# Optimization experiments

Hardware: AMD Instinct MI355X
Metric: run time of the kernel (lower is better)

Reference implementation:

```python
import jax, jax.numpy as jnp
import numpy as np

B, T, D = 2, 2048, 2048
N, KH, H = 16, 8, 128  # query heads, kv heads, head_dim
S = 2048               # cache size
EPS = 1e-6
ROPE_THETA = 1000000.0
K_MASK = -0.7 * float(np.finfo(np.float32).max)  # jax _get_large_negative(float32)


def _rms_norm(x, w):
    rms = jnp.sqrt(jnp.mean(x.astype(jnp.float32) ** 2, axis=-1, keepdims=True) + EPS)
    return (w * x / rms).astype(x.dtype)


def _rope_embeddings(positions, head_dim):
    fraction = jnp.arange(0, head_dim, 2, dtype=jnp.float32) / head_dim
    inv_freq = 1.0 / (ROPE_THETA ** fraction)
    sinusoid = jnp.einsum('BT,k->BTk', positions.astype(jnp.float32), inv_freq,
                          precision=jax.lax.Precision.HIGHEST)
    return jnp.sin(sinusoid), jnp.cos(sinusoid)


def _apply_rope(x, sin, cos):
    h = x.shape[-1] // 2
    x1, x2 = x[..., :h], x[..., h:]
    s, c = sin[:, :, None, :], cos[:, :, None, :]
    return jnp.concatenate([x1 * c - x2 * s, x2 * c + x1 * s], axis=-1).astype(x.dtype)


def _positions_from_segment_ids(seg):
    t = seg.shape[1]
    pos = jnp.arange(t, dtype=jnp.int32)[None, :] - jnp.argmax(seg, axis=1)[:, None]
    return jnp.where(seg != 0, pos, 2 ** 30)


def _num_left_pad(seg):
    return jnp.sum(jnp.cumsum(seg != 0, axis=-1) == 0, axis=-1).astype(jnp.int32)


def _attention(x, q_w, k_w, v_w, o_w, q_norm_w, k_norm_w, k_cache, v_cache,
               segment_ids, start_ind, cur_ind):
    b, t, _ = x.shape
    s = k_cache.shape[1]
    n, kh, h = q_w.shape[1], k_w.shape[1], q_w.shape[2]

    q = _rms_norm(jnp.einsum('BTD,DNH->BTNH', x, q_w), q_norm_w)  # [B,T,N,H]
    k = _rms_norm(jnp.einsum('BSD,DKH->BSKH', x, k_w), k_norm_w)  # [B,T,K,H]
    v = jnp.einsum('BSD,DKH->BSKH', x, v_w)                       # [B,T,K,H]

    start = jnp.where(start_ind < 0, _num_left_pad(segment_ids), start_ind)
    pos = _positions_from_segment_ids(segment_ids) + cur_ind
    sin, cos = _rope_embeddings(pos, h)
    q = _apply_rope(q, sin, cos)
    k = _apply_rope(k, sin, cos)

    # KV-cache update at cur_ind
    k_cache = jax.lax.dynamic_update_slice(k_cache, k, (0, cur_ind, 0, 0))
    v_cache = jax.lax.dynamic_update_slice(v_cache, v, (0, cur_ind, 0, 0))

    # GQA: group query heads per kv head
    qg = q.reshape(b, t, kh, n // kh, h)
    logits = jnp.einsum('BTHGD,BSHD->BHGTS', qg, k_cache) * (h ** -0.5)

    q_pos = cur_ind + jnp.arange(t, dtype=jnp.int32)[None, :] - start[:, None]  # [B,T]
    ts = jnp.arange(s, dtype=jnp.int32)
    kv_seg = (ts[None, :] >= start[:, None]) & (ts[None, :] < cur_ind + t)      # [B,S] bool
    k_pos = ts[None, :] - start[:, None]                                        # [B,S]
    causal = k_pos[:, None, :] <= q_pos[:, :, None]                             # [B,T,S]
    # faithful to original: bool kv segment ids compared against int segment_ids
    seg_mask = kv_seg[:, None, :].astype(segment_ids.dtype) == segment_ids[:, :, None]
    final_mask = (causal & seg_mask)[:, None, None, :, :]                       # [B,1,1,T,S]

    logits = jnp.where(final_mask, logits, K_MASK)
    attn = jax.nn.softmax(logits.astype(jnp.float32), axis=-1).astype(logits.dtype)
    o = jnp.einsum('BHGTS,BSHD->BTHGD', attn, v_cache).reshape(b, t, n, h)
    return jnp.einsum('BTNH,NHD->BTD', o, o_w)


def setup_inputs() -> dict:
    key = jax.random.key(0)
    ks = jax.random.split(key, 5)
    scale = 0.02
    return {
        'x': jax.random.normal(ks[0], (B, T, D), jnp.float32),
        'q_w': jax.random.normal(ks[1], (D, N, H), jnp.float32) * scale,
        'k_w': jax.random.normal(ks[2], (D, KH, H), jnp.float32) * scale,
        'v_w': jax.random.normal(ks[3], (D, KH, H), jnp.float32) * scale,
        'o_w': jax.random.normal(ks[4], (N, H, D), jnp.float32) * scale,
        'q_norm_w': jnp.ones((H,), jnp.float32),
        'k_norm_w': jnp.ones((H,), jnp.float32),
        'k_cache': jnp.zeros((B, S, KH, H), jnp.float32),
        'v_cache': jnp.zeros((B, S, KH, H), jnp.float32),
        'segment_ids': jnp.ones((B, T), jnp.int32),
        'start_ind': jnp.zeros((B,), jnp.int32),
        'cur_ind': 0,
        'right_pads': 0,
    }


def reference(x, q_w, k_w, v_w, o_w, q_norm_w, k_norm_w, k_cache, v_cache,
              segment_ids, start_ind, cur_ind, right_pads):
    # right_pads only advances the cache write pointer (stateful side effect); it
    # does not affect the attention output.
    return _attention(x, q_w, k_w, v_w, o_w, q_norm_w, k_norm_w,
                      k_cache, v_cache, segment_ids, start_ind, cur_ind)
```

## Files before the change

### kernel.cpp

```cpp
#include <hip/hip_runtime.h>
#include <hip/hip_fp16.h>
#include <climits>
#include <math.h>

#define Bc   2
#define Tc   2048
#define Dc   2048
#define Nc   16
#define KHc  8
#define Hc   128
#define Sc   2048

constexpr float EPSc   = 1e-6f;
constexpr float SCALE2 = 0.1275174477984469f;

typedef short short8 __attribute__((ext_vector_type(8)));
typedef _Float16 half8 __attribute__((ext_vector_type(8)));
typedef __fp16 fp16x2 __attribute__((ext_vector_type(2)));
typedef float float4v __attribute__((ext_vector_type(4)));

union U16x8 { uint4 u; short8 s8; half8 h8; unsigned short us[8]; };
union H2U  { fp16x2 h; unsigned u; };
union S8H8 { short8 s; half8 h; };

__device__ __forceinline__ unsigned short f2bf(float f) {
    union { float f; unsigned u; } v; v.f = f;
    unsigned r = v.u + 0x7FFFu + ((v.u >> 16) & 1u);
    return (unsigned short)(r >> 16);
}
__device__ __forceinline__ float bf2f(unsigned short u) {
    union { unsigned u; float f; } v; v.u = ((unsigned)u) << 16;
    return v.f;
}

__device__ __forceinline__ void tc_body(const float* __restrict__ in,
                                        unsigned short* __restrict__ out,
                                        int R, int C, int bx, int by, int tid,
                                        float tile[32][33])
{
    int c0 = bx * 32, r0 = by * 32;
#pragma unroll
    for (int i = 0; i < 4; ++i) {
        int row = (tid >> 5) + i * 8, col = tid & 31;
        tile[row][col] = in[(size_t)(r0 + row) * C + c0 + col];
    }
    __syncthreads();
#pragma unroll
    for (int i = 0; i < 4; ++i) {
        int rowo = (tid >> 5) + i * 8, colo = tid & 31;
        out[(size_t)(c0 + rowo) * R + r0 + colo] = f2bf(tile[colo][rowo]);
    }
}

__global__ __launch_bounds__(256) void prep(const float* __restrict__ x,
                                            const float* __restrict__ qw,
                                            const float* __restrict__ kw,
                                            const float* __restrict__ vw,
                                            const float* __restrict__ ow,
                                            const int* __restrict__ seg,
                                            const int* __restrict__ start_ind,
                                            int* __restrict__ meta,
                                            unsigned short* __restrict__ xb,
                                            unsigned short* __restrict__ qkvwT,
                                            unsigned short* __restrict__ owT)
{
    __shared__ float tile[32][33];
    __shared__ int s_max, s_amax, s_nz;
    int id = blockIdx.x;
    int tid = threadIdx.x;

    if (id < Bc) {
        int b = id;
        if (tid == 0) { s_max = INT_MIN; s_amax = Tc; s_nz = Tc; }
        __syncthreads();
        int lmax = INT_MIN;
        for (int t = tid; t < Tc; t += 256) lmax = max(lmax, seg[b * Tc + t]);
        atomicMax(&s_max, lmax);
        __syncthreads();
        int mv = s_max;
        int lamax = Tc, lnz = Tc;
        for (int t = tid; t < Tc; t += 256) {
            int v = seg[b * Tc + t];
            if (v == mv) lamax = min(lamax, t);
            if (v != 0)  lnz   = min(lnz, t);
        }
        atomicMin(&s_amax, lamax);
        atomicMin(&s_nz, lnz);
        __syncthreads();
        if (tid == 0) {
            meta[b] = s_amax;
            int st = start_ind[b];
            meta[Bc + b] = (st < 0) ? s_nz : st;
        }
        return;
    }
    id -= Bc;
    if (id < 4096) {
        size_t base = ((size_t)id * 256 + tid) * 8;
        float4 a = *(const float4*)&x[base];
        float4 b = *(const float4*)&x[base + 4];
        U16x8 o;
        o.us[0] = f2bf(a.x); o.us[1] = f2bf(a.y); o.us[2] = f2bf(a.z); o.us[3] = f2bf(a.w);
        o.us[4] = f2bf(b.x); o.us[5] = f2bf(b.y); o.us[6] = f2bf(b.z); o.us[7] = f2bf(b.w);
        *(uint4*)&xb[base] = o.u;
        return;
    }
    id -= 4096;
    if (id < 4096) { tc_body(qw, qkvwT, 2048, 2048, id & 63, id >> 6, tid, tile); return; }
    id -= 4096;
    if (id < 2048) { tc_body(kw, qkvwT + (size_t)2048 * 2048, 2048, 1024, id & 31, id >> 5, tid, tile); return; }
    id -= 2048;
    if (id < 2048) { tc_body(vw, qkvwT + (size_t)3072 * 2048, 2048, 1024, id & 31, id >> 5, tid, tile); return; }
    id -= 2048;
    tc_body(ow, owT, 2048, 2048, id & 63, id >> 6, tid, tile);
}

__global__ __launch_bounds__(512, 2) void gemm256(const unsigned short* __restrict__ A,
                                                  const unsigned short* __restrict__ BT,
                                                  void* __restrict__ Cout,
                                                  int M, int N, int K, int out_fp32)
{
    __shared__ __align__(16) unsigned short As[2 * 16384];
    __shared__ __align__(16) unsigned short Bs[2 * 16384];

    int tid = threadIdx.x;
    int lane = tid & 63, w = tid >> 6;
    int quad = lane >> 4, l15 = lane & 15;

    int gx = gridDim.x;
    int nwg = gx * gridDim.y;
    int lin = blockIdx.y * gx + blockIdx.x;
    int swz = (lin & 7) * (nwg >> 3) + (lin >> 3);
    int bm = (swz / gx) * 256, bn = (swz % gx) * 256;

    int KT = K >> 6;

    int colswz = (((lane & 7) ^ ((lane >> 3) & 7)) << 3);
    int r0 = (w * 2) * 8 + (lane >> 3);
    const unsigned short* Ab0 = A + (size_t)(bm + r0) * K + colswz;
    const unsigned short* Bb0 = BT + (size_t)(bn + r0) * K + colswz;
    size_t rowK8 = (size_t)8 * K;
    size_t hK = (size_t)128 * K;

    unsigned short* dA0 = As + (w * 2) * 512;
    unsigned short* dB0 = Bs + (w * 2) * 512;

    auto stA = [&](int kt, int bufp) __attribute__((always_inline)) {
#pragma unroll
        for (int h = 0; h < 2; ++h) {
            __builtin_amdgcn_global_load_lds(
                (__attribute__((address_space(1))) void*)(Ab0 + h * hK + (size_t)kt * 64),
                (__attribute__((address_space(3))) void*)(dA0 + bufp * 16384 + h * 8192), 16, 0, 0);
            __builtin_amdgcn_global_load_lds(
                (__attribute__((address_space(1))) void*)(Ab0 + h * hK + rowK8 + (size_t)kt * 64),
                (__attribute__((address_space(3))) void*)(dA0 + bufp * 16384 + h * 8192 + 512), 16, 0, 0);
        }
    };
    auto stB = [&](int kt, int bufp) __attribute__((always_inline)) {
#pragma unroll
        for (int h = 0; h < 2; ++h) {
            __builtin_amdgcn_global_load_lds(
                (__attribute__((address_space(1))) void*)(Bb0 + h * hK + (size_t)kt * 64),
                (__attribute__((address_space(3))) void*)(dB0 + bufp * 16384 + h * 8192), 16, 0, 0);
            __builtin_amdgcn_global_load_lds(
                (__attribute__((address_space(1))) void*)(Bb0 + h * hK + rowK8 + (size_t)kt * 64),
                (__attribute__((address_space(3))) void*)(dB0 + bufp * 16384 + h * 8192 + 512), 16, 0, 0);
        }
    };

    int ards = (w >> 2) * 8192;
    int brds = (w & 3) * 4096;
    int rowb = l15 * 64;
    int swA = l15 & 7;
    int cof0 = ((quad) ^ swA) << 3;
    int cof1 = ((4 + quad) ^ swA) << 3;

    float4v acc[8][4];
#pragma unroll
    for (int i = 0; i < 8; ++i)
#pragma unroll
        for (int j = 0; j < 4; ++j) acc[i][j] = (float4v)0.f;

    stA(0, 0); stB(0, 0);
    stA(1, 1);
    asm volatile("s_waitcnt vmcnt(4)" ::: "memory");
    __builtin_amdgcn_s_barrier();
    asm volatile("" ::: "memory");

    auto ktile = [&](int kt, int bufp) __attribute__((always_inline)) {
        const unsigned short* ab = As + bufp * 16384 + ards + rowb;
        const unsigned short* bb = Bs + bufp * 16384 + brds + rowb;
        short8 afl[2][4], afh[2][4], bfa[2][2], bfb[2][2];

        if (kt + 1 < KT) stB(kt + 1, bufp ^ 1);
#pragma unroll
        for (int mi = 0; mi < 4; ++mi) {
            afl[0][mi] = *(const short8*)&ab[mi * 1024 + cof0];
            afl[1][mi] = *(const short8*)&ab[mi * 1024 + cof1];
        }
#pragma unroll
        for (int ni = 0; ni < 2; ++ni) {
            bfa[0][ni] = *(const short8*)&bb[ni * 1024 + cof0];
            bfa[1][ni] = *(const short8*)&bb[ni * 1024 + cof1];
        }
        __builtin_amdgcn_s_setprio(1);
#pragma unroll
        for (int kk = 0; kk < 2; ++kk)
#pragma unroll
            for (int mi = 0; mi < 4; ++mi)
#pragma unroll
                for (int ni = 0; ni < 2; ++ni)
                    acc[mi][ni] = __builtin_amdgcn_mfma_f32_16x16x32_bf16(afl[kk][mi], bfa[kk][ni], acc[mi][ni], 0, 0, 0);
        __builtin_amdgcn_s_setprio(0);
#pragma unroll
        for (int ni = 0; ni < 2; ++ni) {
            bfb[0][ni] = *(const short8*)&bb[(2 + ni) * 1024 + cof0];
            bfb[1][ni] = *(const short8*)&bb[(2 + ni) * 1024 + cof1];
        }
        __builtin_amdgcn_s_setprio(1);
#pragma unroll
        for (int kk = 0; kk < 2; ++kk)
#pragma unroll
            for (int mi = 0; mi < 4; ++mi)
#pragma unroll
                for (int ni = 0; ni < 2; ++ni)
                    acc[mi][2 + ni] = __builtin_amdgcn_mfma_f32_16x16x32_bf16(afl[kk][mi], bfb[kk][ni], acc[mi][2 + ni], 0, 0, 0);
        __builtin_amdgcn_s_setprio(0);
#pragma unroll
        for (int mi = 0; mi < 4; ++mi) {
            afh[0][mi] = *(const short8*)&ab[(4 + mi) * 1024 + cof0];
            afh[1][mi] = *(const short8*)&ab[(4 + mi) * 1024 + cof1];
        }
        asm volatile("s_waitcnt lgkmcnt(0)" ::: "memory");
        __builtin_amdgcn_sched_barrier(0);
        __builtin_amdgcn_s_barrier();
        asm volatile("" ::: "memory");

        bool sA = (kt + 2) < KT;
        if (sA) stA(kt + 2, bufp);
        __builtin_amdgcn_s_setprio(1);
#pragma unroll
        for (int kk = 0; kk < 2; ++kk)
#pragma unroll
            for (int mi = 0; mi < 4; ++mi)
#pragma unroll
                for (int ni = 0; ni < 2; ++ni)
                    acc[4 + mi][ni] = __builtin_amdgcn_mfma_f32_16x16x32_bf16(afh[kk][mi], bfa[kk][ni], acc[4 + mi][ni], 0, 0, 0);
#pragma unroll
        for (int kk = 0; kk < 2; ++kk)
#pragma unroll
            for (int mi = 0; mi < 4; ++mi)
#pragma unroll
                for (int ni = 0; ni < 2; ++ni)
                    acc[4 + mi][2 + ni] = __builtin_amdgcn_mfma_f32_16x16x32_bf16(afh[kk][mi], bfb[kk][ni], acc[4 + mi][2 + ni], 0, 0, 0);
        __builtin_amdgcn_s_setprio(0);
        if (sA) asm volatile("s_waitcnt vmcnt(4)" ::: "memory");
        else    asm volatile("s_waitcnt vmcnt(0)" ::: "memory");
        __builtin_amdgcn_sched_barrier(0);
        __builtin_amdgcn_s_barrier();
        asm volatile("" ::: "memory");
    };

    for (int kt = 0; kt < KT; kt += 2) {
        ktile(kt, 0);
        ktile(kt + 1, 1);
    }

    int wm = (w >> 2) * 128, wn = (w & 3) * 64;
#pragma unroll
    for (int mi = 0; mi < 8; ++mi)
#pragma unroll
        for (int ni = 0; ni < 4; ++ni)
#pragma unroll
            for (int reg = 0; reg < 4; ++reg) {
                int row = bm + wm + mi * 16 + quad * 4 + reg;
                int col = bn + wn + ni * 16 + l15;
                float v = acc[mi][ni][reg];
                if (out_fp32) ((float*)Cout)[(size_t)row * N + col] = v;
                else ((unsigned short*)Cout)[(size_t)row * N + col] = f2bf(v);
            }
}

__global__ __launch_bounds__(256) void post(unsigned short* __restrict__ QKVh,
                                            unsigned short* __restrict__ Kall,
                                            unsigned short* __restrict__ Vt,
                                            const float* __restrict__ qw,
                                            const float* __restrict__ kw,
                                            const int* __restrict__ seg,
                                            const int* __restrict__ meta,
                                            const int* __restrict__ cur_ptr,
                                            const float* __restrict__ kc,
                                            const float* __restrict__ vc)
{
    int id = blockIdx.x;
    int tid = threadIdx.x;
    int cur = cur_ptr[0];

    if (id < 24576) {
        int rowid = id * 4 + (tid >> 6);
        int lane = tid & 63;
        int hh = rowid % 24;
        int bt = rowid / 24;
        int t = bt & (Tc - 1);
        int b = bt >> 11;

        const unsigned short* in;
        unsigned short* out;
        const float* wt;
        if (hh < 16) {
            unsigned short* p = QKVh + (size_t)bt * 4096 + hh * Hc;
            in = p; out = p; wt = qw;
        } else {
            int kh = hh - 16;
            in = QKVh + (size_t)bt * 4096 + 2048 + kh * Hc;
            out = Kall + (((size_t)b * Sc + cur + t) * KHc + kh) * Hc;
            wt = kw;
        }
        float v1 = bf2f(in[lane]), v2 = bf2f(in[lane + 64]);
        float ssq = v1 * v1 + v2 * v2;
#pragma unroll
        for (int off = 1; off < 64; off <<= 1) ssq += __shfl_xor(ssq, off);
        float rinv = rsqrtf(ssq * (1.0f / Hc) + EPSc);

        int sg = seg[bt];
        long long pos = (sg != 0) ? (long long)(t - meta[b]) : (long long)(1 << 30);
        float posf = (float)(pos + (long long)cur);
        float inv_freq = exp2f(-(float)lane * (19.931568569324174f / 64.0f));
        float s, c;
        sincosf(posf * inv_freq, &s, &c);

        float n1 = wt[lane] * v1 * rinv;
        float n2 = wt[lane + 64] * v2 * rinv;
        out[lane]      = f2bf(n1 * c - n2 * s);
        out[lane + 64] = f2bf(n2 * c + n1 * s);
        return;
    }
    id -= 24576;
    if (id < 2048) {
        size_t base = ((size_t)id * 256 + tid) * 8;
        int s = (int)((base >> 10) & (Sc - 1));
        if (s >= cur && s < cur + Tc) return;
        float4 a = *(const float4*)&kc[base];
        float4 b = *(const float4*)&kc[base + 4];
        U16x8 o;
        o.us[0] = f2bf(a.x); o.us[1] = f2bf(a.y); o.us[2] = f2bf(a.z); o.us[3] = f2bf(a.w);
        o.us[4] = f2bf(b.x); o.us[5] = f2bf(b.y); o.us[6] = f2bf(b.z); o.us[7] = f2bf(b.w);
        *(uint4*)&Kall[base] = o.u;
        return;
    }
    id -= 2048;
    {
        int gid = id * 256 + tid;
        int h  = gid & 127;
        int s8 = ((gid >> 7) & 255) * 8;
        int kh = (gid >> 15) & 7;
        int b  = gid >> 18;
        int curT = cur + Tc;
        unsigned short tmp[8];
#pragma unroll
        for (int e = 0; e < 8; ++e) {
            int s = s8 + e;
            float f;
            if (s >= cur && s < curT)
                f = bf2f(QKVh[(size_t)(b * Tc + (s - cur)) * 4096 + 3072 + kh * Hc + h]);
            else
                f = vc[((size_t)(b * Sc + s) * KHc + kh) * Hc + h];
            tmp[e] = __half_as_ushort(__float2half(f));
        }
        *(uint4*)&Vt[(((size_t)b * KHc + kh) * Hc + h) * Sc + s8] = *(uint4*)tmp;
    }
}

__global__ __launch_bounds__(512, 4) void flash_mfma(const unsigned short* __restrict__ Qb,
                                                     const unsigned short* __restrict__ Kall,
                                                     const unsigned short* __restrict__ Vt,
                                                     const int* __restrict__ seg,
                                                     const int* __restrict__ meta,
                                                     const int* __restrict__ cur_ptr,
                                                     unsigned short* __restrict__ Ob)
{
    __shared__ __align__(16) unsigned short Ks[64 * 128];
    __shared__ __align__(16) unsigned short Vs[128 * 64];
    __shared__ __align__(16) unsigned short Ps[128 * 64];

    int tid = threadIdx.x;
    int lane = tid & 63, w = tid >> 6;
    int quad = lane >> 4, l15 = lane & 15;
    int bid = blockIdx.x;
    int raw = bid & 15;
    int n  = (bid >> 4) & 15;
    int b  = bid >> 8;
    int qt = (b == 0) ? raw : (15 - raw);
    int kh = n >> 1;
    int cur = cur_ptr[0];
    int startb = meta[Bc + b];
    int curT = cur + Tc;
    int t0 = qt * 128 + w * 16;

    short8 qf[4];
#pragma unroll
    for (int ks = 0; ks < 4; ++ks) {
        int row = t0 + l15;
        U16x8 uq;
        uq.u = *(const uint4*)&Qb[(size_t)(b * Tc + row) * 4096 + n * Hc + ks * 32 + quad * 8];
        qf[ks] = uq.s8;
    }

    int trow0 = t0 + l15;
    int sg0 = seg[b * Tc + trow0];
    int cls = (sg0 == 0) ? 0 : ((sg0 == 1) ? 1 : 2);
    int ct  = cur + trow0;
    unsigned long long mball = __ballot(cls == 1);
    bool allseg1 = (mball == 0xFFFFFFFFFFFFFFFFull);

    float lsum = 0.f;
    float4v oT[8];
#pragma unroll
    for (int i = 0; i < 8; ++i) oT[i] = (float4v)0.f;

    int s_end = min(Sc, cur + qt * 128 + 128);
    int nch = (s_end + 63) >> 6;

    const size_t kstride = (size_t)KHc * Hc;
    const unsigned short* kptr[2];
    unsigned short* kdst[2];
#pragma unroll
    for (int i = 0; i < 2; ++i) {
        int j = w * 2 + i;
        int row = j * 4 + (lane >> 4);
        int pl = lane & 15;
        int pg = pl ^ ((row >> 1) & 7);
        kptr[i] = Kall + (size_t)b * Sc * kstride + (size_t)row * kstride + kh * Hc + pg * 8;
        kdst[i] = Ks + j * 512;
    }
    const unsigned short* vptr[2];
    unsigned short* vdst[2];
#pragma unroll
    for (int i = 0; i < 2; ++i) {
        int j = w * 2 + i;
        int h = j * 8 + (lane >> 3);
        int pl = lane & 7;
        int pg = pl ^ ((h >> 1) & 7);
        vptr[i] = Vt + ((size_t)b * KHc + kh) * (size_t)Hc * Sc + (size_t)h * Sc + pg * 8;
        vdst[i] = Vs + j * 512;
    }
    int sw3 = (l15 >> 1) & 7;
    int sw8 = l15 & 7;
    unsigned short* psrow = Ps + (w * 16 + l15) * 64;

    for (int c = 0; c < nch; ++c) {
        int s0 = c * 64;
#pragma unroll
        for (int i = 0; i < 2; ++i) {
            __builtin_amdgcn_global_load_lds(
                (__attribute__((address_space(1))) void*)(kptr[i] + (size_t)s0 * kstride),
                (__attribute__((address_space(3))) void*)kdst[i], 16, 0, 0);
            __builtin_amdgcn_global_load_lds(
                (__attribute__((address_space(1))) void*)(vptr[i] + s0),
                (__attribute__((address_space(3))) void*)vdst[i], 16, 0, 0);
        }
        __syncthreads();

        float4v st[4];
#pragma unroll
        for (int i = 0; i < 4; ++i) st[i] = (float4v)0.f;
        __builtin_amdgcn_s_setprio(1);
#pragma unroll
        for (int ks = 0; ks < 4; ++ks) {
#pragma unroll
            for (int stile = 0; stile < 4; ++stile) {
                short8 kf = *(const short8*)&Ks[(stile * 16 + l15) * 128 + ((ks * 4 + quad) ^ sw3) * 8];
                st[stile] = __builtin_amdgcn_mfma_f32_16x16x32_bf16(kf, qf[ks], st[stile], 0, 0, 0);
            }
        }
        __builtin_amdgcn_s_setprio(0);

        bool fullok = allseg1 && (s0 >= startb) && (s0 + 63 <= cur + t0) && (s0 + 63 < curT);

#pragma unroll
        for (int stile = 0; stile < 4; ++stile) {
            float p0, p1, p2, p3;
            if (fullok) {
                p0 = exp2f(st[stile][0] * SCALE2);
                p1 = exp2f(st[stile][1] * SCALE2);
                p2 = exp2f(st[stile][2] * SCALE2);
                p3 = exp2f(st[stile][3] * SCALE2);
            } else {
                float pp[4];
#pragma unroll
                for (int reg = 0; reg < 4; ++reg) {
                    int s = s0 + stile * 16 + quad * 4 + reg;
                    int kvseg = (s >= startb && s < curT) ? 1 : 0;
                    bool ok = (s <= ct) && (cls == kvseg);
                    pp[reg] = exp2f(ok ? st[stile][reg] * SCALE2 : -1e30f);
                }
                p0 = pp[0]; p1 = pp[1]; p2 = pp[2]; p3 = pp[3];
            }
            lsum += (p0 + p1) + (p2 + p3);
            H2U a, d;
            a.h = __builtin_amdgcn_cvt_pkrtz(p0, p1);
            d.h = __builtin_amdgcn_cvt_pkrtz(p2, p3);
            uint2 pk; pk.x = a.u; pk.y = d.u;
            *(uint2*)&psrow[(((stile * 2 + (quad >> 1)) ^ sw8) << 3) + (quad & 1) * 4] = pk;
        }

        __builtin_amdgcn_s_setprio(1);
#pragma unroll
        for (int kk = 0; kk < 2; ++kk) {
            S8H8 pf;
            pf.s = *(const short8*)&psrow[((kk * 4 + quad) ^ sw8) << 3];
#pragma unroll
            for (int htile = 0; htile < 8; ++htile) {
                S8H8 vf;
                vf.s = *(const short8*)&Vs[(htile * 16 + l15) * 64 + ((kk * 4 + quad) ^ sw3) * 8];
                oT[htile] = __builtin_amdgcn_mfma_f32_16x16x32_f16(vf.h, pf.h, oT[htile], 0, 0, 0);
            }
        }
        __builtin_amdgcn_s_setprio(0);

        __syncthreads();
    }

    float l = lsum;
    l += __shfl_xor(l, 16);
    l += __shfl_xor(l, 32);
    float linv = (l > 0.f) ? (1.0f / l) : 0.f;

    {
        int trow = t0 + l15;
        size_t base = ((size_t)(b * Tc + trow) * Nc + n) * Hc;
#pragma unroll
        for (int htile = 0; htile < 8; ++htile) {
            float4v v = oT[htile];
            unsigned short r0 = f2bf(v[0] * linv);
            unsigned short r1 = f2bf(v[1] * linv);
            unsigned short r2 = f2bf(v[2] * linv);
            unsigned short r3 = f2bf(v[3] * linv);
            uint2 pk;
            pk.x = (unsigned)r0 | ((unsigned)r1 << 16);
            pk.y = (unsigned)r2 | ((unsigned)r3 << 16);
            *(uint2*)&Ob[base + htile * 16 + quad * 4] = pk;
        }
    }
}

extern "C" void kernel_launch(void* const* d_in, const int* in_sizes, int n_in,
                              void* d_out, int out_size, void* d_ws, size_t ws_size,
                              hipStream_t stream)
{
    const float* x        = (const float*)d_in[0];
    const float* q_w      = (const float*)d_in[1];
    const float* k_w      = (const float*)d_in[2];
    const float* v_w      = (const float*)d_in[3];
    const float* o_w      = (const float*)d_in[4];
    const float* q_norm_w = (const float*)d_in[5];
    const float* k_norm_w = (const float*)d_in[6];
    const float* k_cache  = (const float*)d_in[7];
    const float* v_cache  = (const float*)d_in[8];
    const int*   seg      = (const int*)d_in[9];
    const int*   startind = (const int*)d_in[10];
    const int*   cur_ptr  = (const int*)d_in[11];
    (void)in_sizes; (void)n_in; (void)out_size; (void)ws_size;

    char* base = (char*)d_ws;
    int* meta = (int*)base;
    unsigned short* QKVh = (unsigned short*)(base + 1024);
    unsigned short* Kall = (unsigned short*)(base + 33555456);
    unsigned short* Vt   = (unsigned short*)(base + 41944064);
    unsigned short* xb   = (unsigned short*)(base + 50332672);
    unsigned short* qkvwT= (unsigned short*)(base + 67109888);
    unsigned short* owT  = (unsigned short*)(base + 83887104);
    unsigned short* Ob   = xb;

    prep<<<Bc + 4096 + 4096 + 2048 + 2048 + 4096, 256, 0, stream>>>(
        x, q_w, k_w, v_w, o_w, seg, startind, meta, xb, qkvwT, owT);

    gemm256<<<dim3(16, 16), 512, 0, stream>>>(xb, qkvwT, QKVh, Bc * Tc, 4096, Dc, 0);

    post<<<24576 + 2048 + 2048, 256, 0, stream>>>(QKVh, Kall, Vt,
        q_norm_w, k_norm_w, seg, meta, cur_ptr, k_cache, v_cache);

    flash_mfma<<<Bc * Nc * (Tc / 128), 512, 0, stream>>>(QKVh, Kall, Vt, seg, meta, cur_ptr, Ob);

    gemm256<<<dim3(8, 16), 512, 0, stream>>>(Ob, owT, d_out, Bc * Tc, Dc, Nc * Hc, 1);
}
```

Before: 393.3 us.

## Shrink GEMM tile to 128x128 with 4 waves for more workgroups

Replaces the 256x256, 8-wave GEMM with a 128x128, 4-wave version. Each wave now computes a 64x64 sub-tile, and the LDS staging and fragment loads are restructured to match. Both projection GEMMs launch four times as many workgroups, which improves CU coverage on a 256-CU part: the out-projection previously launched only 128 blocks. The cost is lower arithmetic intensity per tile, so each MFMA needs more global and LDS traffic.

```diff
diff --git a/kernel.cpp b/kernel.cpp
--- a/kernel.cpp
+++ b/kernel.cpp
@@ -115,13 +115,13 @@
     tc_body(ow, owT, 2048, 2048, id & 63, id >> 6, tid, tile);
 }
 
-__global__ __launch_bounds__(512, 2) void gemm256(const unsigned short* __restrict__ A,
+__global__ __launch_bounds__(256, 2) void gemm128(const unsigned short* __restrict__ A,
                                                   const unsigned short* __restrict__ BT,
                                                   void* __restrict__ Cout,
                                                   int M, int N, int K, int out_fp32)
 {
-    __shared__ __align__(16) unsigned short As[2 * 16384];
-    __shared__ __align__(16) unsigned short Bs[2 * 16384];
+    __shared__ __align__(16) unsigned short As[2 * 8192];
+    __shared__ __align__(16) unsigned short Bs[2 * 8192];
 
     int tid = threadIdx.x;
     int lane = tid & 63, w = tid >> 6;
@@ -131,53 +131,44 @@
     int nwg = gx * gridDim.y;
     int lin = blockIdx.y * gx + blockIdx.x;
     int swz = (lin & 7) * (nwg >> 3) + (lin >> 3);
-    int bm = (swz / gx) * 256, bn = (swz % gx) * 256;
+    int bm = (swz / gx) * 128, bn = (swz % gx) * 128;
 
     int KT = K >> 6;
 
     int colswz = (((lane & 7) ^ ((lane >> 3) & 7)) << 3);
-    int r0 = (w * 2) * 8 + (lane >> 3);
-    const unsigned short* Ab0 = A + (size_t)(bm + r0) * K + colswz;
-    const unsigned short* Bb0 = BT + (size_t)(bn + r0) * K + colswz;
+    int r0 = w * 32 + (lane >> 3);
+    const unsigned short* Ab = A + (size_t)(bm + r0) * K + colswz;
+    const unsigned short* Bb = BT + (size_t)(bn + r0) * K + colswz;
     size_t rowK8 = (size_t)8 * K;
-    size_t hK = (size_t)128 * K;
-
-    unsigned short* dA0 = As + (w * 2) * 512;
-    unsigned short* dB0 = Bs + (w * 2) * 512;
+
+    unsigned short* dA = As + w * 2048;
+    unsigned short* dB = Bs + w * 2048;
 
     auto stA = [&](int kt, int bufp) __attribute__((always_inline)) {
 #pragma unroll
-        for (int h = 0; h < 2; ++h) {
+        for (int i = 0; i < 4; ++i)
             __builtin_amdgcn_global_load_lds(
-                (__attribute__((address_space(1))) void*)(Ab0 + h * hK + (size_t)kt * 64),
-                (__attribute__((address_space(3))) void*)(dA0 + bufp * 16384 + h * 8192), 16, 0, 0);
-            __builtin_amdgcn_global_load_lds(
-                (__attribute__((address_space(1))) void*)(Ab0 + h * hK + rowK8 + (size_t)kt * 64),
-                (__attribute__((address_space(3))) void*)(dA0 + bufp * 16384 + h * 8192 + 512), 16, 0, 0);
-        }
+                (__attribute__((address_space(1))) void*)(Ab + (size_t)i * rowK8 + (size_t)kt * 64),
+                (__attribute__((address_space(3))) void*)(dA + bufp * 8192 + i * 512), 16, 0, 0);
     };
     auto stB = [&](int kt, int bufp) __attribute__((always_inline)) {
 #pragma unroll
-        for (int h = 0; h < 2; ++h) {
+        for (int i = 0; i < 4; ++i)
             __builtin_amdgcn_global_load_lds(
-                (__attribute__((address_space(1))) void*)(Bb0 + h * hK + (size_t)kt * 64),
-                (__attribute__((address_space(3))) void*)(dB0 + bufp * 16384 + h * 8192), 16, 0, 0);
-            __builtin_amdgcn_global_load_lds(
-                (__attribute__((address_space(1))) void*)(Bb0 + h * hK + rowK8 + (size_t)kt * 64),
-                (__attribute__((address_space(3))) void*)(dB0 + bufp * 16384 + h * 8192 + 512), 16, 0, 0);
-        }
+                (__attribute__((address_space(1))) void*)(Bb + (size_t)i * rowK8 + (size_t)kt * 64),
+                (__attribute__((address_space(3))) void*)(dB + bufp * 8192 + i * 512), 16, 0, 0);
     };
 
-    int ards = (w >> 2) * 8192;
-    int brds = (w & 3) * 4096;
-    int rowb = l15 * 64;
-    int swA = l15 & 7;
-    int cof0 = ((quad) ^ swA) << 3;
-    int cof1 = ((4 + quad) ^ swA) << 3;
-
-    float4v acc[8][4];
-#pragma unroll
-    for (int i = 0; i < 8; ++i)
+    int wm = (w >> 1) * 64, wn = (w & 1) * 64;
+    int swk = l15 & 7;
+    int cof0 = ((quad) ^ swk) << 3;
+    int cof1 = ((4 + quad) ^ swk) << 3;
+    const int arow = (wm + l15) * 64;
+    const int brow = (wn + l15) * 64;
+
+    float4v acc[4][4];
+#pragma unroll
+    for (int i = 0; i < 4; ++i)
 #pragma unroll
         for (int j = 0; j < 4; ++j) acc[i][j] = (float4v)0.f;
 
@@ -188,20 +179,20 @@
     asm volatile("" ::: "memory");
 
     auto ktile = [&](int kt, int bufp) __attribute__((always_inline)) {
-        const unsigned short* ab = As + bufp * 16384 + ards + rowb;
-        const unsigned short* bb = Bs + bufp * 16384 + brds + rowb;
-        short8 afl[2][4], afh[2][4], bfa[2][2], bfb[2][2];
+        const unsigned short* ab = As + bufp * 8192 + arow;
+        const unsigned short* bb = Bs + bufp * 8192 + brow;
+        short8 af[2][4], bf[2][4];
 
         if (kt + 1 < KT) stB(kt + 1, bufp ^ 1);
 #pragma unroll
         for (int mi = 0; mi < 4; ++mi) {
-            afl[0][mi] = *(const short8*)&ab[mi * 1024 + cof0];
-            afl[1][mi] = *(const short8*)&ab[mi * 1024 + cof1];
-        }
-#pragma unroll
-        for (int ni = 0; ni < 2; ++ni) {
-            bfa[0][ni] = *(const short8*)&bb[ni * 1024 + cof0];
-            bfa[1][ni] = *(const short8*)&bb[ni * 1024 + cof1];
+            af[0][mi] = *(const short8*)&ab[mi * 1024 + cof0];
+            af[1][mi] = *(const short8*)&ab[mi * 1024 + cof1];
+        }
+#pragma unroll
+        for (int ni = 0; ni < 4; ++ni) {
+            bf[0][ni] = *(const short8*)&bb[ni * 1024 + cof0];
+            bf[1][ni] = *(const short8*)&bb[ni * 1024 + cof1];
         }
         __builtin_amdgcn_s_setprio(1);
 #pragma unroll
@@ -210,27 +201,8 @@
             for (int mi = 0; mi < 4; ++mi)
 #pragma unroll
                 for (int ni = 0; ni < 2; ++ni)
-                    acc[mi][ni] = __builtin_amdgcn_mfma_f32_16x16x32_bf16(afl[kk][mi], bfa[kk][ni], acc[mi][ni], 0, 0, 0);
+                    acc[mi][ni] = __builtin_amdgcn_mfma_f32_16x16x32_bf16(af[kk][mi], bf[kk][ni], acc[mi][ni], 0, 0, 0);
         __builtin_amdgcn_s_setprio(0);
-#pragma unroll
-        for (int ni = 0; ni < 2; ++ni) {
-            bfb[0][ni] = *(const short8*)&bb[(2 + ni) * 1024 + cof0];
-            bfb[1][ni] = *(const short8*)&bb[(2 + ni) * 1024 + cof1];
-        }
-        __builtin_amdgcn_s_setprio(1);
-#pragma unroll
-        for (int kk = 0; kk < 2; ++kk)
-#pragma unroll
-            for (int mi = 0; mi < 4; ++mi)
-#pragma unroll
-                for (int ni = 0; ni < 2; ++ni)
-                    acc[mi][2 + ni] = __builtin_amdgcn_mfma_f32_16x16x32_bf16(afl[kk][mi], bfb[kk][ni], acc[mi][2 + ni], 0, 0, 0);
-        __builtin_amdgcn_s_setprio(0);
-#pragma unroll
-        for (int mi = 0; mi < 4; ++mi) {
-            afh[0][mi] = *(const short8*)&ab[(4 + mi) * 1024 + cof0];
-            afh[1][mi] = *(const short8*)&ab[(4 + mi) * 1024 + cof1];
-        }
         asm volatile("s_waitcnt lgkmcnt(0)" ::: "memory");
         __builtin_amdgcn_sched_barrier(0);
         __builtin_amdgcn_s_barrier();
@@ -244,15 +216,8 @@
 #pragma unroll
             for (int mi = 0; mi < 4; ++mi)
 #pragma unroll
-                for (int ni = 0; ni < 2; ++ni)
-                    acc[4 + mi][ni] = __builtin_amdgcn_mfma_f32_16x16x32_bf16(afh[kk][mi], bfa[kk][ni], acc[4 + mi][ni], 0, 0, 0);
-#pragma unroll
-        for (int kk = 0; kk < 2; ++kk)
-#pragma unroll
-            for (int mi = 0; mi < 4; ++mi)
-#pragma unroll
-                for (int ni = 0; ni < 2; ++ni)
-                    acc[4 + mi][2 + ni] = __builtin_amdgcn_mfma_f32_16x16x32_bf16(afh[kk][mi], bfb[kk][ni], acc[4 + mi][2 + ni], 0, 0, 0);
+                for (int ni = 2; ni < 4; ++ni)
+                    acc[mi][ni] = __builtin_amdgcn_mfma_f32_16x16x32_bf16(af[kk][mi], bf[kk][ni], acc[mi][ni], 0, 0, 0);
         __builtin_amdgcn_s_setprio(0);
         if (sA) asm volatile("s_waitcnt vmcnt(4)" ::: "memory");
         else    asm volatile("s_waitcnt vmcnt(0)" ::: "memory");
@@ -266,9 +231,8 @@
         ktile(kt + 1, 1);
     }
 
-    int wm = (w >> 2) * 128, wn = (w & 3) * 64;
-#pragma unroll
-    for (int mi = 0; mi < 8; ++mi)
+#pragma unroll
+    for (int mi = 0; mi < 4; ++mi)
 #pragma unroll
         for (int ni = 0; ni < 4; ++ni)
 #pragma unroll
@@ -575,12 +539,12 @@
     prep<<<Bc + 4096 + 4096 + 2048 + 2048 + 4096, 256, 0, stream>>>(
         x, q_w, k_w, v_w, o_w, seg, startind, meta, xb, qkvwT, owT);
 
-    gemm256<<<dim3(16, 16), 512, 0, stream>>>(xb, qkvwT, QKVh, Bc * Tc, 4096, Dc, 0);
+    gemm128<<<dim3(32, 32), 256, 0, stream>>>(xb, qkvwT, QKVh, Bc * Tc, 4096, Dc, 0);
 
     post<<<24576 + 2048 + 2048, 256, 0, stream>>>(QKVh, Kall, Vt,
         q_norm_w, k_norm_w, seg, meta, cur_ptr, k_cache, v_cache);
 
     flash_mfma<<<Bc * Nc * (Tc / 128), 512, 0, stream>>>(QKVh, Kall, Vt, seg, meta, cur_ptr, Ob);
 
-    gemm256<<<dim3(8, 16), 512, 0, stream>>>(Ob, owT, d_out, Bc * Tc, Dc, Nc * Hc, 1);
-}
+    gemm128<<<dim3(16, 32), 256, 0, stream>>>(Ob, owT, d_out, Bc * Tc, Dc, Nc * Hc, 1);
+}
```

Result: faster. 380.9 us (-3.1%).
